# Kernel optimization log

Measured on AMD Instinct MI355X. Metric: run time of the kernel, lower is better.

The kernel has to match this reference:

```python
import jax, jax.numpy as jnp
import numpy as np

N = 4096
D = 256
NUM_LAYERS = 20
NUM_QKV = NUM_LAYERS * 10  # 200


def setup_inputs() -> dict:
    key = jax.random.key(0)
    ks = jax.random.split(key, 12)
    s = 1.0 / np.sqrt(D)
    return {
        "x": jax.random.normal(ks[0], (N, D), jnp.float32),
        "Wq": jax.random.normal(ks[1], (NUM_QKV, D, D), jnp.float32) * s,
        "bq": jax.random.normal(ks[2], (NUM_QKV, D), jnp.float32) * s,
        "Wk": jax.random.normal(ks[3], (NUM_QKV, D, D), jnp.float32) * s,
        "bk": jax.random.normal(ks[4], (NUM_QKV, D), jnp.float32) * s,
        "Wv": jax.random.normal(ks[5], (NUM_QKV, D, D), jnp.float32) * s,
        "bv": jax.random.normal(ks[6], (NUM_QKV, D), jnp.float32) * s,
        "Wl": jax.random.normal(ks[7], (NUM_LAYERS, D, D), jnp.float32) * s,
        "bl": jax.random.normal(ks[8], (NUM_LAYERS, D), jnp.float32) * s,
        "final_weight": jax.random.normal(ks[9], (D, D), jnp.float32),
        "final_bias": jax.random.normal(ks[10], (D,), jnp.float32),
    }


def reference(x, Wq, bq, Wk, bk, Wv, bv, Wl, bl, final_weight, final_bias):
    d = x.shape[1]
    scale = jnp.asarray(1.0 / np.sqrt(d), x.dtype)

    # Stream the 200 independent attention blocks with scan, accumulating the sum
    # so only one [N, N] score matrix is live at a time.
    def attn_step(acc, p):
        wq, bq_, wk, bk_, wv, bv_ = p
        Q = x @ wq.T + bq_            # [N, d]  (nn.Linear: x @ W.T + b)
        K = x @ wk.T + bk_
        V = x @ wv.T + bv_
        scores = jax.nn.sigmoid((Q @ K.T) * scale)   # [N, N]
        weights = jax.nn.softmax(scores, axis=1)
        return acc + weights @ V, None

    acc, _ = jax.lax.scan(attn_step, jnp.zeros_like(x), (Wq, bq, Wk, bk, Wv, bv))
    out = acc / jnp.asarray(Wq.shape[0], x.dtype)    # mean over num_qkv blocks

    def mlp_step(h, p):
        w, b = p
        return jax.nn.relu(h @ w.T + b), None

    out, _ = jax.lax.scan(mlp_step, out, (Wl, bl))
    out = jax.nn.sigmoid(out @ final_weight) + final_bias
    return out  # squeeze(-1) is a no-op for d_model > 1
```

## Files before the change

kernel.cpp:

```cpp
#include <hip/hip_runtime.h>

typedef unsigned short u16;
typedef __attribute__((ext_vector_type(8))) short s16x8;
typedef __attribute__((ext_vector_type(4))) short s16x4;
typedef __attribute__((ext_vector_type(4))) float f32x4;
typedef __attribute__((ext_vector_type(16))) float f32x16;
typedef __attribute__((ext_vector_type(4))) int i32x4;

#define MFMA16(a, b, c) __builtin_amdgcn_mfma_f32_16x16x32_bf16(a, b, c, 0, 0, 0)
#define MFMA32(a, b, c) __builtin_amdgcn_mfma_f32_32x32x16_bf16(a, b, c, 0, 0, 0)
#define EXP2(x) __builtin_amdgcn_exp2f(x)

__device__ __forceinline__ u16 f2bf(float f) {
  unsigned u = __float_as_uint(f);
  u += 0x7FFFu + ((u >> 16) & 1u);
  return (u16)(u >> 16);
}

__device__ __forceinline__ void async_cp16(const u16* g, u16* l) {
  __builtin_amdgcn_global_load_lds(
      (__attribute__((address_space(1))) void*)g,
      (__attribute__((address_space(3))) void*)l,
      16, 0, 0);
}

__global__ void cvt4(const float* __restrict__ s, u16* __restrict__ d, int n4) {
  int i = blockIdx.x * 256 + threadIdx.x;
  if (i >= n4) return;
  f32x4 v = *(const f32x4*)(s + 4L * i);
  s16x4 o;
  o[0] = (short)f2bf(v[0]); o[1] = (short)f2bf(v[1]);
  o[2] = (short)f2bf(v[2]); o[3] = (short)f2bf(v[3]);
  *(s16x4*)(d + 4L * i) = o;
}

__global__ void cvt_t(const float* __restrict__ s, u16* __restrict__ d) {
  int j = blockIdx.x, k = threadIdx.x;
  d[j * 256 + k] = f2bf(s[k * 256 + j]);
}

__global__ __launch_bounds__(256, 4) void gemm_qkv(
    const u16* __restrict__ xb, const u16* __restrict__ wq, const u16* __restrict__ wk,
    const u16* __restrict__ wv, const float* __restrict__ bqv,
    const float* __restrict__ bkv, const float* __restrict__ bvv,
    u16* __restrict__ qkv, int c0) {
  __shared__ __align__(16) u16 lds[16384];
  const int z = blockIdx.z, g = blockIdx.y;
  const u16* A; const u16* B; const float* bias; u16* out;
  int tiles_n, Nb;
  if (z == 0)      { A = xb; B = wq + (long)(c0 + g) * 65536; bias = bqv + (long)(c0 + g) * 256;
                     out = qkv + (long)g * 3145728;           tiles_n = 2;  Nb = 256; }
  else if (z == 1) { A = xb; B = wk + (long)(c0 + g) * 65536; bias = bkv + (long)(c0 + g) * 256;
                     out = qkv + (long)g * 3145728 + 1048576; tiles_n = 2;  Nb = 256; }
  else             { A = wv + (long)(c0 + g) * 65536; B = xb; bias = bvv + (long)(c0 + g) * 256;
                     out = qkv + (long)g * 3145728 + 2097152; tiles_n = 32; Nb = 4096; }

  const int tid = threadIdx.x;
  const int lane = tid & 63;
  const int l15 = lane & 15, q4 = lane >> 4;
  const int w = tid >> 6;
  const int qm = w >> 1, qn = w & 1;
  const int tm = blockIdx.x / tiles_n, tn = blockIdx.x % tiles_n;
  const int row0 = tm << 7, col0 = tn << 7;

  f32x4 C[4][4];
#pragma unroll
  for (int i = 0; i < 4; ++i)
#pragma unroll
    for (int j = 0; j < 4; ++j) C[i][j] = (f32x4)0.0f;

  u16* Al = lds;
  u16* Bl = lds + 8192;

  for (int kc = 0; kc < 4; ++kc) {
    __syncthreads();
#pragma unroll
    for (int i = 0; i < 4; ++i) {
      int s = tid + i * 256;
      int r = s >> 3, p = s & 7;
      async_cp16(A + (long)(row0 + r) * 256 + kc * 64 + ((p ^ (r & 7)) << 3), Al + s * 8);
    }
#pragma unroll
    for (int i = 0; i < 4; ++i) {
      int s = tid + i * 256;
      int r = s >> 3, p = s & 7;
      async_cp16(B + (long)(col0 + r) * 256 + kc * 64 + ((p ^ (r & 7)) << 3), Bl + s * 8);
    }
    __syncthreads();
#pragma unroll
    for (int ks = 0; ks < 2; ++ks) {
      s16x8 a[4];
#pragma unroll
      for (int mt = 0; mt < 4; ++mt) {
        int r = qm * 64 + mt * 16 + l15;
        int kb = ks * 4 + q4;
        a[mt] = *(const s16x8*)(Al + r * 64 + ((kb ^ (r & 7)) << 3));
      }
#pragma unroll
      for (int nt = 0; nt < 4; ++nt) {
        int rn = qn * 64 + nt * 16 + l15;
        int kb = ks * 4 + q4;
        s16x8 b = *(const s16x8*)(Bl + rn * 64 + ((kb ^ (rn & 7)) << 3));
#pragma unroll
        for (int mt = 0; mt < 4; ++mt) C[mt][nt] = MFMA16(a[mt], b, C[mt][nt]);
      }
    }
  }

  const int gr0 = row0 + qm * 64, gc0 = col0 + qn * 64;
  if (z < 2) {
    const float sc = (z == 0) ? 0.090168440f : 1.0f;
#pragma unroll
    for (int nt = 0; nt < 4; ++nt) {
      int cc = gc0 + nt * 16 + l15;
      float bc = bias[cc];
#pragma unroll
      for (int mt = 0; mt < 4; ++mt)
#pragma unroll
        for (int e = 0; e < 4; ++e) {
          int rr = gr0 + mt * 16 + q4 * 4 + e;
          out[(long)rr * 256 + cc] = f2bf((C[mt][nt][e] + bc) * sc);
        }
    }
  } else {
    float bm[4][4];
#pragma unroll
    for (int mt = 0; mt < 4; ++mt)
#pragma unroll
      for (int e = 0; e < 4; ++e) bm[mt][e] = bias[gr0 + mt * 16 + q4 * 4 + e];
#pragma unroll
    for (int nt = 0; nt < 4; ++nt) {
      int cc = gc0 + nt * 16 + l15;
#pragma unroll
      for (int mt = 0; mt < 4; ++mt)
#pragma unroll
        for (int e = 0; e < 4; ++e) {
          int rr = gr0 + mt * 16 + q4 * 4 + e;
          long ad = (long)(cc >> 5) * 8192 + ((cc >> 3) & 3) * 2048 + rr * 8 + (cc & 7);
          out[ad] = f2bf(C[mt][nt][e] + bm[mt][e]);
        }
    }
  }
}

template <int MODE>
__global__ __launch_bounds__(256, 4) void gemm_bt(
    const u16* __restrict__ A, const u16* __restrict__ B, void* __restrict__ Cout,
    const float* __restrict__ bias) {
  __shared__ __align__(16) u16 lds[16384];
  const int tid = threadIdx.x;
  const int lane = tid & 63;
  const int l15 = lane & 15, q4 = lane >> 4;
  const int w = tid >> 6;
  const int qm = w >> 1, qn = w & 1;
  const int tm = blockIdx.x >> 1, tn = blockIdx.x & 1;
  const int row0 = tm << 7, col0 = tn << 7;

  f32x4 C[4][4];
#pragma unroll
  for (int i = 0; i < 4; ++i)
#pragma unroll
    for (int j = 0; j < 4; ++j) C[i][j] = (f32x4)0.0f;

  u16* Al = lds;
  u16* Bl = lds + 8192;

  for (int kc = 0; kc < 4; ++kc) {
    __syncthreads();
#pragma unroll
    for (int i = 0; i < 4; ++i) {
      int s = tid + i * 256;
      int r = s >> 3, p = s & 7;
      async_cp16(A + (long)(row0 + r) * 256 + kc * 64 + ((p ^ (r & 7)) << 3), Al + s * 8);
    }
#pragma unroll
    for (int i = 0; i < 4; ++i) {
      int s = tid + i * 256;
      int r = s >> 3, p = s & 7;
      async_cp16(B + (long)(col0 + r) * 256 + kc * 64 + ((p ^ (r & 7)) << 3), Bl + s * 8);
    }
    __syncthreads();
#pragma unroll
    for (int ks = 0; ks < 2; ++ks) {
      s16x8 a[4];
#pragma unroll
      for (int mt = 0; mt < 4; ++mt) {
        int r = qm * 64 + mt * 16 + l15;
        int kb = ks * 4 + q4;
        a[mt] = *(const s16x8*)(Al + r * 64 + ((kb ^ (r & 7)) << 3));
      }
#pragma unroll
      for (int nt = 0; nt < 4; ++nt) {
        int rn = qn * 64 + nt * 16 + l15;
        int kb = ks * 4 + q4;
        s16x8 b = *(const s16x8*)(Bl + rn * 64 + ((kb ^ (rn & 7)) << 3));
#pragma unroll
        for (int mt = 0; mt < 4; ++mt) C[mt][nt] = MFMA16(a[mt], b, C[mt][nt]);
      }
    }
  }

  const int gr0 = row0 + qm * 64, gc0 = col0 + qn * 64;
#pragma unroll
  for (int nt = 0; nt < 4; ++nt) {
    int cc = gc0 + nt * 16 + l15;
    float bc = bias[cc];
#pragma unroll
    for (int mt = 0; mt < 4; ++mt)
#pragma unroll
      for (int e = 0; e < 4; ++e) {
        int rr = gr0 + mt * 16 + q4 * 4 + e;
        float v = C[mt][nt][e];
        if (MODE == 2) {
          v = fmaxf(v + bc, 0.0f);
          ((u16*)Cout)[(long)rr * 256 + cc] = f2bf(v);
        } else {
          v = 1.0f / (1.0f + __expf(-v)) + bc;
          ((float*)Cout)[(long)rr * 256 + cc] = v;
        }
      }
  }
}

__global__ __launch_bounds__(256, 2) void attn(const u16* __restrict__ qkv,
                                               float* __restrict__ acc, int gc, int swiz) {
  __shared__ __align__(16) u16 lds[32768];

  const int f = blockIdx.x;
  int b, tile;
  if (swiz) { b = (f & 7) + ((f >> 8) << 3); tile = (f >> 3) & 31; }
  else { b = f >> 5; tile = f & 31; }
  if (b >= gc) return;

  const int tid = threadIdx.x;
  const int lane = tid & 63, w = tid >> 6;
  const int l31 = lane & 31, h = lane >> 5;
  const long slot = 3145728L * b;
  const u16* Qg = qkv + slot;
  const u16* Kg = qkv + slot + 1048576;
  const u16* Vg = qkv + slot + 2097152;
  const int rw = tile * 128 + w * 32;

  const int krow = tid >> 3;
  const int ksw = (tid & 7) ^ (krow & 7);

  int koff[4];
#pragma unroll
  for (int j = 0; j < 4; ++j)
    koff[j] = l31 * 64 + ((((j << 1) | h) ^ (l31 & 7)) << 3);
  const int voff = h * 2048 + l31 * 8;

  s16x8 qf[16];
  {
    const u16* qr = Qg + (long)(rw + l31) * 256 + h * 8;
#pragma unroll
    for (int ks = 0; ks < 16; ++ks) qf[ks] = *(const s16x8*)(qr + ks * 16);
  }

  f32x16 O[8];
#pragma unroll
  for (int nt = 0; nt < 8; ++nt) O[nt] = (f32x16)0.0f;
  float rs = 0.0f;

#pragma unroll
  for (int i = 0; i < 4; ++i)
    async_cp16(Kg + krow * 256 + ((i * 8 + ksw) << 3), lds + (tid + i * 256) * 8);
#pragma unroll
  for (int i = 0; i < 4; ++i)
    async_cp16(Vg + (tid + i * 256) * 8, lds + 16384 + (tid + i * 256) * 8);

  for (int jt = 0; jt < 128; ++jt) {
    const int cb = (jt & 1) << 13;
    const u16* Kc = lds + cb;
    const u16* Vc = lds + 16384 + cb;
    __syncthreads();

    if (jt < 127) {
      const u16* Kn = Kg + (jt + 1) * 8192;
      const u16* Vn = Vg + (jt + 1) * 8192;
      u16* Kd = lds + (cb ^ 8192);
      u16* Vd = lds + 16384 + (cb ^ 8192);
#pragma unroll
      for (int i = 0; i < 4; ++i)
        async_cp16(Kn + krow * 256 + ((i * 8 + ksw) << 3), Kd + (tid + i * 256) * 8);
#pragma unroll
      for (int i = 0; i < 4; ++i)
        async_cp16(Vn + (tid + i * 256) * 8, Vd + (tid + i * 256) * 8);
    }

    f32x16 S = (f32x16)0.0f;
#pragma unroll
    for (int ks = 0; ks < 16; ++ks) {
      s16x8 kf = *(const s16x8*)(Kc + (ks >> 2) * 2048 + koff[ks & 3]);
      S = MFMA32(kf, qf[ks], S);
    }

    float p[16];
#pragma unroll
    for (int r = 0; r < 16; ++r) {
      float u = EXP2(-S[r]);
      float sg = __builtin_amdgcn_rcpf(1.0f + u);
      p[r] = EXP2(sg * 1.44269504f);
      rs += p[r];
    }

    int pk[8];
#pragma unroll
    for (int i = 0; i < 8; ++i)
      asm("v_cvt_pk_bf16_f32 %0, %1, %2"
          : "=v"(pk[i]) : "v"(p[2 * i]), "v"(p[2 * i + 1]));

    auto r02 = __builtin_amdgcn_permlane32_swap(pk[0], pk[2], false, false);
    auto r13 = __builtin_amdgcn_permlane32_swap(pk[1], pk[3], false, false);
    auto r46 = __builtin_amdgcn_permlane32_swap(pk[4], pk[6], false, false);
    auto r57 = __builtin_amdgcn_permlane32_swap(pk[5], pk[7], false, false);
    union { i32x4 i; s16x8 v; } a0u, a1u;
    a0u.i[0] = (int)r02[0]; a0u.i[1] = (int)r13[0];
    a0u.i[2] = (int)r02[1]; a0u.i[3] = (int)r13[1];
    a1u.i[0] = (int)r46[0]; a1u.i[1] = (int)r57[0];
    a1u.i[2] = (int)r46[1]; a1u.i[3] = (int)r57[1];

#pragma unroll
    for (int nt = 0; nt < 8; ++nt) {
      s16x8 v0 = *(const s16x8*)(Vc + voff + nt * 256);
      s16x8 v1 = *(const s16x8*)(Vc + voff + 4096 + nt * 256);
      O[nt] = MFMA32(a0u.v, v0, O[nt]);
      O[nt] = MFMA32(a1u.v, v1, O[nt]);
    }
  }

  float tot = rs + __shfl(rs, lane ^ 32, 64);
#pragma unroll
  for (int r = 0; r < 16; ++r) {
    int qr = (r & 3) + 8 * (r >> 2) + 4 * h;
    float ls = __shfl(tot, qr, 64);
    float scn = 0.005f * __builtin_amdgcn_rcpf(ls);
#pragma unroll
    for (int nt = 0; nt < 8; ++nt)
      unsafeAtomicAdd(acc + (long)(rw + qr) * 256 + nt * 32 + l31, O[nt][r] * scn);
  }
}

extern "C" void kernel_launch(void* const* d_in, const int* in_sizes, int n_in,
                              void* d_out, int out_size, void* d_ws, size_t ws_size,
                              hipStream_t stream) {
  const float* x = (const float*)d_in[0];
  const float* Wq = (const float*)d_in[1];
  const float* bq = (const float*)d_in[2];
  const float* Wk = (const float*)d_in[3];
  const float* bk = (const float*)d_in[4];
  const float* Wv = (const float*)d_in[5];
  const float* bv = (const float*)d_in[6];
  const float* Wl = (const float*)d_in[7];
  const float* bl = (const float*)d_in[8];
  const float* fw = (const float*)d_in[9];
  const float* fb = (const float*)d_in[10];
  float* out = (float*)d_out;

  u16* wsb = (u16*)d_ws;
  u16* xb = wsb;
  u16* wqb = wsb + 1048576;
  u16* wkb = wqb + 13107200;
  u16* wvb = wkb + 13107200;
  u16* wlb = wvb + 13107200;
  u16* fwtb = wlb + 1310720;
  u16* h0 = fwtb + 65536;
  u16* h1 = h0 + 1048576;
  u16* qkvb = h1 + 1048576;

  long fixedBytes = (long)((char*)qkvb - (char*)wsb);
  long avail = (long)ws_size - fixedBytes;
  int G = (int)(avail / 6291456L);
  if (G > 16) G = 16;
  if (G < 1) G = 1;

  hipMemsetAsync(d_out, 0, (size_t)out_size * sizeof(float), stream);

  cvt4<<<dim3(1024), 256, 0, stream>>>(x, xb, 262144);
  cvt4<<<dim3(12800), 256, 0, stream>>>(Wq, wqb, 3276800);
  cvt4<<<dim3(12800), 256, 0, stream>>>(Wk, wkb, 3276800);
  cvt4<<<dim3(12800), 256, 0, stream>>>(Wv, wvb, 3276800);
  cvt4<<<dim3(1280), 256, 0, stream>>>(Wl, wlb, 327680);
  cvt_t<<<dim3(256), 256, 0, stream>>>(fw, fwtb);

  for (int c0 = 0; c0 < 200; c0 += G) {
    int gc = (200 - c0 < G) ? (200 - c0) : G;
    gemm_qkv<<<dim3(64, gc, 3), 256, 0, stream>>>(xb, wqb, wkb, wvb, bq, bk, bv, qkvb, c0);
    int swiz = (gc == 16 || gc == 8) ? 1 : 0;
    attn<<<dim3(32 * gc), 256, 0, stream>>>(qkvb, out, gc, swiz);
  }

  cvt4<<<dim3(1024), 256, 0, stream>>>(out, h0, 262144);
  for (int i = 0; i < 20; ++i) {
    u16* hin = (i & 1) ? h1 : h0;
    u16* hout = (i & 1) ? h0 : h1;
    gemm_bt<2><<<dim3(64), 256, 0, stream>>>(hin, wlb + (long)i * 65536, hout,
                                             bl + (long)i * 256);
  }
  gemm_bt<3><<<dim3(64), 256, 0, stream>>>(h0, fwtb, d_out, fb);
}
```

Measured before the change: 4.450 ms.

## Use FP8 Q/K for attention scores and software-pipeline QK with PV

Q and K are now written by the projection GEMM as FP8, with scale factors folded into the epilogue and K stored in a swizzled layout. Attention computes scores with FP8 MFMA. The loop is restructured so the QK product for the next tile is issued alongside the PV MFMAs of the current tile, with separate double-buffering for K and V and raised wave priority. This halves Q/K memory and LDS traffic and is meant to overlap score computation with the softmax/PV phase, at the cost of FP8 precision loss in the scores.

Result: faster. 4.351 ms (-2.2%).

```diff
diff --git a/kernel.cpp b/kernel.cpp
--- a/kernel.cpp
+++ b/kernel.cpp
@@ -1,6 +1,7 @@
 #include <hip/hip_runtime.h>
 
 typedef unsigned short u16;
+typedef unsigned char u8;
 typedef __attribute__((ext_vector_type(8))) short s16x8;
 typedef __attribute__((ext_vector_type(4))) short s16x4;
 typedef __attribute__((ext_vector_type(4))) float f32x4;
@@ -9,6 +10,7 @@
 
 #define MFMA16(a, b, c) __builtin_amdgcn_mfma_f32_16x16x32_bf16(a, b, c, 0, 0, 0)
 #define MFMA32(a, b, c) __builtin_amdgcn_mfma_f32_32x32x16_bf16(a, b, c, 0, 0, 0)
+#define MFMA32F8(a, b, c) __builtin_amdgcn_mfma_f32_32x32x16_fp8_fp8(a, b, c, 0, 0, 0)
 #define EXP2(x) __builtin_amdgcn_exp2f(x)
 
 __device__ __forceinline__ u16 f2bf(float f) {
@@ -17,7 +19,12 @@
   return (u16)(u >> 16);
 }
 
-__device__ __forceinline__ void async_cp16(const u16* g, u16* l) {
+__device__ __forceinline__ u8 f2fp8(float f) {
+  int r = __builtin_amdgcn_cvt_pk_fp8_f32(f, f, 0, false);
+  return (u8)(r & 0xff);
+}
+
+__device__ __forceinline__ void async_cp16(const void* g, void* l) {
   __builtin_amdgcn_global_load_lds(
       (__attribute__((address_space(1))) void*)g,
       (__attribute__((address_space(3))) void*)l,
@@ -43,17 +50,17 @@
     const u16* __restrict__ xb, const u16* __restrict__ wq, const u16* __restrict__ wk,
     const u16* __restrict__ wv, const float* __restrict__ bqv,
     const float* __restrict__ bkv, const float* __restrict__ bvv,
-    u16* __restrict__ qkv, int c0) {
+    u8* __restrict__ qkv, int c0) {
   __shared__ __align__(16) u16 lds[16384];
   const int z = blockIdx.z, g = blockIdx.y;
-  const u16* A; const u16* B; const float* bias; u16* out;
-  int tiles_n, Nb;
+  const u16* A; const u16* B; const float* bias; u8* outb;
+  int tiles_n;
   if (z == 0)      { A = xb; B = wq + (long)(c0 + g) * 65536; bias = bqv + (long)(c0 + g) * 256;
-                     out = qkv + (long)g * 3145728;           tiles_n = 2;  Nb = 256; }
+                     outb = qkv + (long)g * 4194304;           tiles_n = 2; }
   else if (z == 1) { A = xb; B = wk + (long)(c0 + g) * 65536; bias = bkv + (long)(c0 + g) * 256;
-                     out = qkv + (long)g * 3145728 + 1048576; tiles_n = 2;  Nb = 256; }
+                     outb = qkv + (long)g * 4194304 + 1048576; tiles_n = 2; }
   else             { A = wv + (long)(c0 + g) * 65536; B = xb; bias = bvv + (long)(c0 + g) * 256;
-                     out = qkv + (long)g * 3145728 + 2097152; tiles_n = 32; Nb = 4096; }
+                     outb = qkv + (long)g * 4194304 + 2097152; tiles_n = 32; }
 
   const int tid = threadIdx.x;
   const int lane = tid & 63;
@@ -108,8 +115,8 @@
   }
 
   const int gr0 = row0 + qm * 64, gc0 = col0 + qn * 64;
-  if (z < 2) {
-    const float sc = (z == 0) ? 0.090168440f : 1.0f;
+  if (z == 0) {
+    const float sc = 0.36067376f;
 #pragma unroll
     for (int nt = 0; nt < 4; ++nt) {
       int cc = gc0 + nt * 16 + l15;
@@ -119,10 +126,28 @@
 #pragma unroll
         for (int e = 0; e < 4; ++e) {
           int rr = gr0 + mt * 16 + q4 * 4 + e;
-          out[(long)rr * 256 + cc] = f2bf((C[mt][nt][e] + bc) * sc);
+          outb[(long)rr * 256 + cc] = f2fp8((C[mt][nt][e] + bc) * sc);
         }
     }
+  } else if (z == 1) {
+    const float sc = 0.25f;
+#pragma unroll
+    for (int nt = 0; nt < 4; ++nt) {
+      int cc = gc0 + nt * 16 + l15;
+      float bc = bias[cc];
+      int cid = ((cc >> 5) << 1) | ((cc >> 3) & 1);
+      int byt = ((cc >> 4) & 1) * 8 + (cc & 7);
+#pragma unroll
+      for (int mt = 0; mt < 4; ++mt)
+#pragma unroll
+        for (int e = 0; e < 4; ++e) {
+          int key = gr0 + mt * 16 + q4 * 4 + e;
+          outb[(long)key * 256 + ((cid ^ (key & 7)) << 4) + byt] =
+              f2fp8((C[mt][nt][e] + bc) * sc);
+        }
+    }
   } else {
+    u16* out = (u16*)outb;
     float bm[4][4];
 #pragma unroll
     for (int mt = 0; mt < 4; ++mt)
@@ -222,9 +247,9 @@
   }
 }
 
-__global__ __launch_bounds__(256, 2) void attn(const u16* __restrict__ qkv,
+__global__ __launch_bounds__(256, 2) void attn(const u8* __restrict__ qkv,
                                                float* __restrict__ acc, int gc, int swiz) {
-  __shared__ __align__(16) u16 lds[32768];
+  __shared__ __align__(16) u8 ldsb[49152];
 
   const int f = blockIdx.x;
   int b, tile;
@@ -235,26 +260,21 @@
   const int tid = threadIdx.x;
   const int lane = tid & 63, w = tid >> 6;
   const int l31 = lane & 31, h = lane >> 5;
-  const long slot = 3145728L * b;
-  const u16* Qg = qkv + slot;
-  const u16* Kg = qkv + slot + 1048576;
-  const u16* Vg = qkv + slot + 2097152;
+  const long slot = 4194304L * b;
+  const u8* Qg = qkv + slot;
+  const u8* Kg = qkv + slot + 1048576;
+  const u8* Vg = qkv + slot + 2097152;
   const int rw = tile * 128 + w * 32;
 
-  const int krow = tid >> 3;
-  const int ksw = (tid & 7) ^ (krow & 7);
-
-  int koff[4];
-#pragma unroll
-  for (int j = 0; j < 4; ++j)
-    koff[j] = l31 * 64 + ((((j << 1) | h) ^ (l31 & 7)) << 3);
+  const int kb256 = l31 * 256;
+  const int xk = l31 & 7;
   const int voff = h * 2048 + l31 * 8;
 
-  s16x8 qf[16];
+  long qf[16];
   {
-    const u16* qr = Qg + (long)(rw + l31) * 256 + h * 8;
-#pragma unroll
-    for (int ks = 0; ks < 16; ++ks) qf[ks] = *(const s16x8*)(qr + ks * 16);
+    const u8* qr = Qg + (long)(rw + l31) * 256 + h * 8;
+#pragma unroll
+    for (int ks = 0; ks < 16; ++ks) qf[ks] = *(const long*)(qr + ks * 16);
   }
 
   f32x16 O[8];
@@ -263,38 +283,26 @@
   float rs = 0.0f;
 
 #pragma unroll
+  for (int i = 0; i < 2; ++i)
+    async_cp16(Kg + (tid + i * 256) * 16, ldsb + (tid + i * 256) * 16);
+#pragma unroll
   for (int i = 0; i < 4; ++i)
-    async_cp16(Kg + krow * 256 + ((i * 8 + ksw) << 3), lds + (tid + i * 256) * 8);
-#pragma unroll
-  for (int i = 0; i < 4; ++i)
-    async_cp16(Vg + (tid + i * 256) * 8, lds + 16384 + (tid + i * 256) * 8);
+    async_cp16(Vg + (tid + i * 256) * 16, ldsb + 16384 + (tid + i * 256) * 16);
+#pragma unroll
+  for (int i = 0; i < 2; ++i)
+    async_cp16(Kg + 8192 + (tid + i * 256) * 16, ldsb + 8192 + (tid + i * 256) * 16);
+  __syncthreads();
+
+  f32x16 S = (f32x16)0.0f;
+#pragma unroll
+  for (int r = 0; r < 8; ++r) {
+    i32x4 kv = *(const i32x4*)(ldsb + kb256 + ((((r << 1) | h) ^ xk) << 4));
+    union { i32x4 v4; long l2[2]; } ku; ku.v4 = kv;
+    S = MFMA32F8(ku.l2[0], qf[2 * r], S);
+    S = MFMA32F8(ku.l2[1], qf[2 * r + 1], S);
+  }
 
   for (int jt = 0; jt < 128; ++jt) {
-    const int cb = (jt & 1) << 13;
-    const u16* Kc = lds + cb;
-    const u16* Vc = lds + 16384 + cb;
-    __syncthreads();
-
-    if (jt < 127) {
-      const u16* Kn = Kg + (jt + 1) * 8192;
-      const u16* Vn = Vg + (jt + 1) * 8192;
-      u16* Kd = lds + (cb ^ 8192);
-      u16* Vd = lds + 16384 + (cb ^ 8192);
-#pragma unroll
-      for (int i = 0; i < 4; ++i)
-        async_cp16(Kn + krow * 256 + ((i * 8 + ksw) << 3), Kd + (tid + i * 256) * 8);
-#pragma unroll
-      for (int i = 0; i < 4; ++i)
-        async_cp16(Vn + (tid + i * 256) * 8, Vd + (tid + i * 256) * 8);
-    }
-
-    f32x16 S = (f32x16)0.0f;
-#pragma unroll
-    for (int ks = 0; ks < 16; ++ks) {
-      s16x8 kf = *(const s16x8*)(Kc + (ks >> 2) * 2048 + koff[ks & 3]);
-      S = MFMA32(kf, qf[ks], S);
-    }
-
     float p[16];
 #pragma unroll
     for (int r = 0; r < 16; ++r) {
@@ -303,13 +311,11 @@
       p[r] = EXP2(sg * 1.44269504f);
       rs += p[r];
     }
-
     int pk[8];
 #pragma unroll
     for (int i = 0; i < 8; ++i)
       asm("v_cvt_pk_bf16_f32 %0, %1, %2"
           : "=v"(pk[i]) : "v"(p[2 * i]), "v"(p[2 * i + 1]));
-
     auto r02 = __builtin_amdgcn_permlane32_swap(pk[0], pk[2], false, false);
     auto r13 = __builtin_amdgcn_permlane32_swap(pk[1], pk[3], false, false);
     auto r46 = __builtin_amdgcn_permlane32_swap(pk[4], pk[6], false, false);
@@ -320,13 +326,47 @@
     a1u.i[0] = (int)r46[0]; a1u.i[1] = (int)r57[0];
     a1u.i[2] = (int)r46[1]; a1u.i[3] = (int)r57[1];
 
-#pragma unroll
-    for (int nt = 0; nt < 8; ++nt) {
-      s16x8 v0 = *(const s16x8*)(Vc + voff + nt * 256);
-      s16x8 v1 = *(const s16x8*)(Vc + voff + 4096 + nt * 256);
-      O[nt] = MFMA32(a0u.v, v0, O[nt]);
-      O[nt] = MFMA32(a1u.v, v1, O[nt]);
-    }
+    __syncthreads();
+
+    if (jt < 126) {
+      const u8* src = Kg + (long)(jt + 2) * 8192;
+      u8* dst = ldsb + ((jt & 1) << 13);
+#pragma unroll
+      for (int i = 0; i < 2; ++i)
+        async_cp16(src + (tid + i * 256) * 16, dst + (tid + i * 256) * 16);
+    }
+    if (jt < 127) {
+      const u8* src = Vg + (long)(jt + 1) * 16384;
+      u8* dst = ldsb + 16384 + (((jt + 1) & 1) << 14);
+#pragma unroll
+      for (int i = 0; i < 4; ++i)
+        async_cp16(src + (tid + i * 256) * 16, dst + (tid + i * 256) * 16);
+    }
+
+    __builtin_amdgcn_s_setprio(1);
+    if (jt < 127) {
+      const u8* Kc = ldsb + (((jt + 1) & 1) << 13);
+      f32x16 Sn = (f32x16)0.0f;
+#pragma unroll
+      for (int r = 0; r < 8; ++r) {
+        i32x4 kv = *(const i32x4*)(Kc + kb256 + ((((r << 1) | h) ^ xk) << 4));
+        union { i32x4 v4; long l2[2]; } ku; ku.v4 = kv;
+        Sn = MFMA32F8(ku.l2[0], qf[2 * r], Sn);
+        Sn = MFMA32F8(ku.l2[1], qf[2 * r + 1], Sn);
+      }
+      S = Sn;
+    }
+    {
+      const u16* Vc = (const u16*)(ldsb + 16384 + ((jt & 1) << 14));
+#pragma unroll
+      for (int nt = 0; nt < 8; ++nt) {
+        s16x8 v0 = *(const s16x8*)(Vc + voff + nt * 256);
+        s16x8 v1 = *(const s16x8*)(Vc + voff + 4096 + nt * 256);
+        O[nt] = MFMA32(a0u.v, v0, O[nt]);
+        O[nt] = MFMA32(a1u.v, v1, O[nt]);
+      }
+    }
+    __builtin_amdgcn_s_setprio(0);
   }
 
   float tot = rs + __shfl(rs, lane ^ 32, 64);
@@ -366,11 +406,11 @@
   u16* fwtb = wlb + 1310720;
   u16* h0 = fwtb + 65536;
   u16* h1 = h0 + 1048576;
-  u16* qkvb = h1 + 1048576;
+  u8* qkvb = (u8*)(h1 + 1048576);
 
   long fixedBytes = (long)((char*)qkvb - (char*)wsb);
   long avail = (long)ws_size - fixedBytes;
-  int G = (int)(avail / 6291456L);
+  int G = (int)(avail / 4194304L);
   if (G > 16) G = 16;
   if (G < 1) G = 1;
 
```
